# Optimization experiments

Hardware: AMD Instinct MI355X
Metric: run time of the kernel (lower is better)

## Reference

```python
import jax, jax.numpy as jnp
import numpy as np

T, B, A_DIM = 64, 128, 5
N_AGENTS, N_CAP = 8, 7
OBS_D = 64
CAP_D = N_AGENTS * N_CAP  # 56
FC, HN, TGT = 128, 128, 64
D = N_CAP + 1  # transformer model dim = 8
NH, FF, NL = 4, 64, 2
EPS = 1e-6


def _ln(x, s, b):
    m = jnp.mean(x, -1, keepdims=True)
    v = jnp.mean(jnp.square(x - m), -1, keepdims=True)
    return (x - m) * jax.lax.rsqrt(v + EPS) * s + b


def _hyper(x, w1, b1, w2, b2):
    return jax.nn.relu(x @ w1 + b1) @ w2 + b2


def setup_inputs() -> dict:
    key = jax.random.key(0)
    ks = iter(jax.random.split(key, 40))

    def rn(shape, s=0.1):
        return jax.random.normal(next(ks), shape, jnp.float32) * s

    return dict(
        hidden=jnp.zeros((B, FC), jnp.float32),
        full_obs=jax.random.normal(next(ks), (T, B, OBS_D + CAP_D), jnp.float32),
        dones=jax.random.randint(next(ks), (T, B), 0, 2, jnp.int32),
        embed_w=rn((OBS_D, FC)), embed_b=jnp.zeros((FC,), jnp.float32),
        gru_wi=rn((FC, 3 * FC)), gru_wh=rn((FC, 3 * FC)), gru_bh=jnp.zeros((3 * FC,), jnp.float32),
        tWq=rn((NL, D, D), 0.3), tWk=rn((NL, D, D), 0.3), tWv=rn((NL, D, D), 0.3), tWo=rn((NL, D, D), 0.3),
        ln1_s=jnp.ones((NL, D), jnp.float32), ln1_b=jnp.zeros((NL, D), jnp.float32),
        ffw1=rn((NL, D, FF), 0.2), ffb1=jnp.zeros((NL, FF), jnp.float32),
        ffw2=rn((NL, FF, D), 0.2), ffb2=jnp.zeros((NL, D), jnp.float32),
        ln2_s=jnp.ones((NL, D), jnp.float32), ln2_b=jnp.zeros((NL, D), jnp.float32),
        hw1_1=rn((D, HN)), hb1_1=jnp.zeros((HN,), jnp.float32), hw2_1=rn((HN, FC * TGT), 0.02), hb2_1=jnp.zeros((FC * TGT,), jnp.float32),
        hw1_2=rn((D, HN)), hb1_2=jnp.zeros((HN,), jnp.float32), hw2_2=rn((HN, TGT), 0.02), hb2_2=jnp.zeros((TGT,), jnp.float32),
        hw1_3=rn((D, HN)), hb1_3=jnp.zeros((HN,), jnp.float32), hw2_3=rn((HN, TGT * A_DIM), 0.01), hb2_3=jnp.zeros((TGT * A_DIM,), jnp.float32),
        hw1_4=rn((D, HN)), hb1_4=jnp.zeros((HN,), jnp.float32), hw2_4=rn((HN, A_DIM), 0.01), hb2_4=jnp.zeros((A_DIM,), jnp.float32),
    )


def reference(hidden, full_obs, dones, embed_w, embed_b, gru_wi, gru_wh, gru_bh,
              tWq, tWk, tWv, tWo, ln1_s, ln1_b, ffw1, ffb1, ffw2, ffb2, ln2_s, ln2_b,
              hw1_1, hb1_1, hw2_1, hb2_1, hw1_2, hb1_2, hw2_2, hb2_2,
              hw1_3, hb1_3, hw2_3, hb2_3, hw1_4, hb1_4, hw2_4, hb2_4):
    obs = full_obs[:, :, :OBS_D]          # [T,B,OBS_D]
    cap = full_obs[:, :, OBS_D:]          # [T,B,CAP_D]
    emb = jax.nn.relu(obs @ embed_w + embed_b)  # [T,B,FC]
    resets = dones.astype(bool)

    # --- GRU scan over time (flax GRUCell math: input dense no bias, hidden dense with bias) ---
    def gru_step(h, xt):
        e, d = xt
        h = jnp.where(d[:, None], 0.0, h)
        gi = e @ gru_wi                   # [B, 3*FC]
        gh = h @ gru_wh + gru_bh
        ir, iz, inn = jnp.split(gi, 3, -1)
        hr, hz, hn = jnp.split(gh, 3, -1)
        r = jax.nn.sigmoid(ir + hr)
        z = jax.nn.sigmoid(iz + hz)
        n = jnp.tanh(inn + r * hn)
        hnew = (1.0 - z) * n + z * h
        return hnew, hnew

    hidden, emb_seq = jax.lax.scan(gru_step, hidden, (emb, resets))

    # --- transformer over agents dim ---
    x = cap.reshape(T * B, N_AGENTS, N_CAP)
    flag = jnp.zeros((T * B, N_AGENTS, 1), jnp.float32).at[:, 0, 0].set(1.0)
    x = jnp.concatenate([x, flag], axis=-1)   # [N, A, D]
    hd = D // NH
    scale = 1.0 / jnp.sqrt(jnp.float32(hd))
    for l in range(NL):
        q = (x @ tWq[l]).reshape(-1, N_AGENTS, NH, hd)
        k = (x @ tWk[l]).reshape(-1, N_AGENTS, NH, hd)
        v = (x @ tWv[l]).reshape(-1, N_AGENTS, NH, hd)
        att = jax.nn.softmax(jnp.einsum('nqhd,nkhd->nhqk', q, k) * scale, axis=-1)
        o = jnp.einsum('nhqk,nkhd->nqhd', att, v).reshape(-1, N_AGENTS, D) @ tWo[l]
        # original does x = norm(attn + x); x = x + dropout(x) -> doubles x
        x = 2.0 * _ln(o + x, ln1_s[l], ln1_b[l])
        ff = jax.nn.relu(x @ ffw1[l] + ffb1[l]) @ ffw2[l] + ffb2[l]
        x = 2.0 * _ln(ff + x, ln2_s[l], ln2_b[l])
    cap_repr = jnp.mean(x, axis=1).reshape(T, B, D)

    # --- hypernetworks -> per-(t,b) weights ---
    w1 = _hyper(cap_repr, hw1_1, hb1_1, hw2_1, hb2_1).reshape(T, B, FC, TGT)
    b1 = _hyper(cap_repr, hw1_2, hb1_2, hw2_2, hb2_2).reshape(T, B, 1, TGT)
    w2 = _hyper(cap_repr, hw1_3, hb1_3, hw2_3, hb2_3).reshape(T, B, TGT, A_DIM)
    b2 = _hyper(cap_repr, hw1_4, hb1_4, hw2_4, hb2_4).reshape(T, B, 1, A_DIM)

    h1 = jax.nn.relu(emb_seq[:, :, None, :] @ w1 + b1)   # [T,B,1,TGT]
    logits = (h1 @ w2 + b2).squeeze(2)                    # [T,B,A_DIM]
    return hidden, logits
```

## Files before the change

### kernel.cpp

```cpp
#include <hip/hip_runtime.h>
#include <hip/hip_bf16.h>
#include <stdint.h>

#define TT 64
#define BB 128
#define OBSD 64
#define FOBS 120
#define FC 128
#define G3 384
#define NS 8192
#define DD 8
#define FF 64
#define HN 128
#define TGT 64
#define ADIM 5

typedef __attribute__((ext_vector_type(8))) short bf16x8;
typedef __attribute__((ext_vector_type(4))) float f32x4;

__device__ __forceinline__ float sigmoidf_(float x) { return 1.0f / (1.0f + __expf(-x)); }
__device__ __forceinline__ float tanhf_(float x) {
    float e = __expf(-2.0f * fabsf(x));
    float r = (1.0f - e) / (1.0f + e);
    return copysignf(r, x);
}
__device__ __forceinline__ unsigned short f2bf_rne(float x) {
    unsigned u = __float_as_uint(x);
    return (unsigned short)((u + 0x7fffu + ((u >> 16) & 1u)) >> 16);
}

__global__ __launch_bounds__(256) void k_embed(
    const float* __restrict__ fobs, const float* __restrict__ We,
    const float* __restrict__ be, float* __restrict__ emb)
{
    __shared__ float obs_t[64][68];
    __shared__ float W_t[64][128];
    int tid = threadIdx.x;
    int s0 = blockIdx.x * 64;
    {
        int rl = tid >> 4, e4 = tid & 15;
#pragma unroll
        for (int rr = 0; rr < 4; ++rr) {
            int r = rl + rr * 16;
            float4 v = *(const float4*)&fobs[(size_t)(s0 + r) * FOBS + e4 * 4];
            *(float4*)&obs_t[r][e4 * 4] = v;
        }
    }
#pragma unroll
    for (int i = 0; i < 8; ++i) {
        int idx = tid + i * 256;
        int e = idx >> 5, c4 = idx & 31;
        float4 v = *(const float4*)&We[(size_t)e * 128 + c4 * 4];
        *(float4*)&W_t[e][c4 * 4] = v;
    }
    __syncthreads();
    int c = tid & 127, half = tid >> 7;
    float acc[32];
    float bc = be[c];
#pragma unroll
    for (int k = 0; k < 32; ++k) acc[k] = bc;
#pragma unroll
    for (int e4 = 0; e4 < 16; ++e4) {
        float w0 = W_t[4 * e4 + 0][c], w1 = W_t[4 * e4 + 1][c];
        float w2 = W_t[4 * e4 + 2][c], w3 = W_t[4 * e4 + 3][c];
#pragma unroll
        for (int k = 0; k < 32; ++k) {
            float4 ov = *(const float4*)&obs_t[half * 32 + k][e4 * 4];
            acc[k] += ov.x * w0 + ov.y * w1 + ov.z * w2 + ov.w * w3;
        }
    }
#pragma unroll
    for (int k = 0; k < 32; ++k)
        emb[(size_t)(s0 + half * 32 + k) * FC + c] = fmaxf(acc[k], 0.0f);
}

__global__ __launch_bounds__(256) void k_gi(
    const float* __restrict__ emb, const float* __restrict__ Wi, float* __restrict__ gi)
{
    __shared__ float e_t[64][132];
    __shared__ float w_t[128 * 64];
    int tid = threadIdx.x;
    int st = blockIdx.x / 6, gt = blockIdx.x % 6;
    int s0 = st * 64, g0 = gt * 64;
#pragma unroll
    for (int i = 0; i < 8; ++i) {
        int idx = tid + i * 256;
        int r = idx >> 5, c4 = idx & 31;
        float4 v = *(const float4*)&emb[(size_t)(s0 + r) * FC + c4 * 4];
        *(float4*)&e_t[r][c4 * 4] = v;
    }
#pragma unroll
    for (int i = 0; i < 8; ++i) {
        int idx = tid + i * 256;
        int r = idx >> 4, g4 = idx & 15;
        float4 v = *(const float4*)&Wi[(size_t)r * G3 + g0 + g4 * 4];
        *(float4*)&w_t[r * 64 + g4 * 4] = v;
    }
    __syncthreads();
    int sb4 = (tid >> 4) * 4, ob4 = (tid & 15) * 4;
    float acc[4][4];
#pragma unroll
    for (int a = 0; a < 4; ++a)
#pragma unroll
        for (int b = 0; b < 4; ++b) acc[a][b] = 0.0f;
    for (int c4 = 0; c4 < 32; ++c4) {
        float4 e4[4], w4[4];
#pragma unroll
        for (int si = 0; si < 4; ++si) e4[si] = *(const float4*)&e_t[sb4 + si][c4 * 4];
#pragma unroll
        for (int cc = 0; cc < 4; ++cc) w4[cc] = *(const float4*)&w_t[(c4 * 4 + cc) * 64 + ob4];
#pragma unroll
        for (int si = 0; si < 4; ++si) {
            const float* ep = (const float*)&e4[si];
#pragma unroll
            for (int cc = 0; cc < 4; ++cc) {
                float ev = ep[cc];
                const float* wp = (const float*)&w4[cc];
                acc[si][0] += ev * wp[0];
                acc[si][1] += ev * wp[1];
                acc[si][2] += ev * wp[2];
                acc[si][3] += ev * wp[3];
            }
        }
    }
#pragma unroll
    for (int si = 0; si < 4; ++si) {
        float4 sv;
        sv.x = acc[si][0]; sv.y = acc[si][1]; sv.z = acc[si][2]; sv.w = acc[si][3];
        *(float4*)&gi[(size_t)(s0 + sb4 + si) * G3 + g0 + ob4] = sv;
    }
}

__global__ __launch_bounds__(256) void k_prepW(
    const float* __restrict__ W, unsigned short* __restrict__ W_swz)
{
    int fid = blockIdx.x * 256 + threadIdx.x;
    int lane = fid & 63;
    int nt = (fid >> 6) & 3;
    int ks = (fid >> 8) & 3;
    int j  = fid >> 10;
    int col = nt * 16 + (lane & 15);
    int kbase = ks * 32 + ((lane >> 4) * 8);
    const float* src = W + ((size_t)j * 128 + kbase) * 64 + col;
    unsigned short o[8];
#pragma unroll
    for (int i = 0; i < 8; ++i) o[i] = f2bf_rne(src[(size_t)i * 64]);
    *(uint4*)&W_swz[(size_t)fid * 8] = *(const uint4*)o;
}

__global__ __launch_bounds__(768) void k_gru(
    const float* __restrict__ gi, const float* __restrict__ Wh, const float* __restrict__ bh,
    const int* __restrict__ dones, const float* __restrict__ h0,
    float* __restrict__ emb_seq, unsigned short* __restrict__ embb,
    float* __restrict__ hid_out)
{
    __shared__ float h_lds[128];
    __shared__ float gh_lds[384];
    int b = blockIdx.x, tid = threadIdx.x;
    int col = tid >> 1, half = tid & 1;
    float W[64];
#pragma unroll
    for (int i = 0; i < 64; ++i) W[i] = Wh[(size_t)(half * 64 + i) * G3 + col];
    float bias = bh[col];
    if (tid < 128) h_lds[tid] = h0[(size_t)b * FC + tid];
    __syncthreads();
    for (int t = 0; t < TT; ++t) {
        float hs = dones[t * BB + b] ? 0.0f : 1.0f;
        float d = 0.0f;
#pragma unroll
        for (int i4 = 0; i4 < 16; ++i4) {
            float4 h4 = *(const float4*)&h_lds[half * 64 + i4 * 4];
            d += W[i4 * 4 + 0] * h4.x + W[i4 * 4 + 1] * h4.y
               + W[i4 * 4 + 2] * h4.z + W[i4 * 4 + 3] * h4.w;
        }
        d *= hs;
        d += __shfl_xor(d, 1, 64);
        if (half == 0) gh_lds[col] = d + bias;
        __syncthreads();
        if (tid < 128) {
            int c = tid;
            const float* gr = gi + ((size_t)t * BB + b) * G3;
            float r = sigmoidf_(gr[c] + gh_lds[c]);
            float z = sigmoidf_(gr[128 + c] + gh_lds[128 + c]);
            float n = tanhf_(gr[256 + c] + r * gh_lds[256 + c]);
            float hnew = (1.0f - z) * n + z * (hs * h_lds[c]);
            h_lds[c] = hnew;
            emb_seq[((size_t)t * BB + b) * FC + c] = hnew;
            embb[((size_t)t * BB + b) * FC + c] = f2bf_rne(hnew);
        }
        __syncthreads();
    }
    if (tid < 128) hid_out[(size_t)b * FC + tid] = h_lds[tid];
}

__global__ __launch_bounds__(256) void k_attn(
    const float* __restrict__ fobs,
    const float* __restrict__ tWq, const float* __restrict__ tWk,
    const float* __restrict__ tWv, const float* __restrict__ tWo,
    const float* __restrict__ ln1s, const float* __restrict__ ln1b,
    const float* __restrict__ ffw1, const float* __restrict__ ffb1,
    const float* __restrict__ ffw2, const float* __restrict__ ffb2,
    const float* __restrict__ ln2s, const float* __restrict__ ln2b,
    float* __restrict__ cap_repr)
{
    __shared__ float wq[2][8][8], wk[2][8][8], wv[2][8][8], wo[2][8][8];
    __shared__ float l1s[2][8], l1b[2][8], l2s[2][8], l2b[2][8];
    __shared__ float f1[2][8][64], fb1[2][64];
    __shared__ float f2[2][64][8], fb2w[2][8];
    __shared__ float k_l[32][8][9], v_l[32][8][9];
    int tid = threadIdx.x;
    for (int i = tid; i < 128; i += 256) {
        ((float*)wq)[i] = tWq[i]; ((float*)wk)[i] = tWk[i];
        ((float*)wv)[i] = tWv[i]; ((float*)wo)[i] = tWo[i];
        ((float*)fb1)[i] = ffb1[i];
    }
    if (tid < 16) {
        ((float*)l1s)[tid] = ln1s[tid]; ((float*)l1b)[tid] = ln1b[tid];
        ((float*)l2s)[tid] = ln2s[tid]; ((float*)l2b)[tid] = ln2b[tid];
        ((float*)fb2w)[tid] = ffb2[tid];
    }
    for (int i = tid; i < 1024; i += 256) { ((float*)f1)[i] = ffw1[i]; ((float*)f2)[i] = ffw2[i]; }
    int sl = tid >> 3, a = tid & 7;
    int s = blockIdx.x * 32 + sl;
    float x[8];
#pragma unroll
    for (int i = 0; i < 7; ++i) x[i] = fobs[(size_t)s * FOBS + OBSD + a * 7 + i];
    x[7] = (a == 0) ? 1.0f : 0.0f;
    __syncthreads();
    for (int l = 0; l < 2; ++l) {
        float q[8], k[8], v[8];
#pragma unroll
        for (int d = 0; d < 8; ++d) { q[d] = 0.f; k[d] = 0.f; v[d] = 0.f; }
#pragma unroll
        for (int e = 0; e < 8; ++e) {
            float xe = x[e];
#pragma unroll
            for (int d = 0; d < 8; ++d) {
                q[d] += xe * wq[l][e][d];
                k[d] += xe * wk[l][e][d];
                v[d] += xe * wv[l][e][d];
            }
        }
#pragma unroll
        for (int d = 0; d < 8; ++d) { k_l[sl][a][d] = k[d]; v_l[sl][a][d] = v[d]; }
        __syncthreads();
        float o[8];
#pragma unroll
        for (int h = 0; h < 4; ++h) {
            float sc[8]; float mx = -1e30f;
#pragma unroll
            for (int ka = 0; ka < 8; ++ka) {
                float sv = (q[2 * h] * k_l[sl][ka][2 * h] + q[2 * h + 1] * k_l[sl][ka][2 * h + 1])
                           * 0.70710678118654752f;
                sc[ka] = sv; mx = fmaxf(mx, sv);
            }
            float ssum = 0.f;
#pragma unroll
            for (int ka = 0; ka < 8; ++ka) { sc[ka] = __expf(sc[ka] - mx); ssum += sc[ka]; }
            float inv = 1.0f / ssum;
            float o0 = 0.f, o1 = 0.f;
#pragma unroll
            for (int ka = 0; ka < 8; ++ka) {
                float at = sc[ka] * inv;
                o0 += at * v_l[sl][ka][2 * h];
                o1 += at * v_l[sl][ka][2 * h + 1];
            }
            o[2 * h] = o0; o[2 * h + 1] = o1;
        }
        float y[8];
#pragma unroll
        for (int e = 0; e < 8; ++e) y[e] = x[e];
#pragma unroll
        for (int d = 0; d < 8; ++d) {
            float od = o[d];
#pragma unroll
            for (int e = 0; e < 8; ++e) y[e] += od * wo[l][d][e];
        }
        {
            float m = 0.f;
#pragma unroll
            for (int e = 0; e < 8; ++e) m += y[e];
            m *= 0.125f;
            float vv = 0.f;
#pragma unroll
            for (int e = 0; e < 8; ++e) { float dd = y[e] - m; vv += dd * dd; }
            vv *= 0.125f;
            float rs = rsqrtf(vv + 1e-6f);
#pragma unroll
            for (int e = 0; e < 8; ++e)
                x[e] = 2.0f * ((y[e] - m) * rs * l1s[l][e] + l1b[l][e]);
        }
        float t1[64];
#pragma unroll
        for (int f = 0; f < 64; ++f) t1[f] = 0.f;
#pragma unroll
        for (int e = 0; e < 8; ++e) {
            float xe = x[e];
#pragma unroll
            for (int f = 0; f < 64; ++f) t1[f] += xe * f1[l][e][f];
        }
        float y2[8];
#pragma unroll
        for (int e = 0; e < 8; ++e) y2[e] = x[e] + fb2w[l][e];
#pragma unroll
        for (int f = 0; f < 64; ++f) {
            float tf = fmaxf(t1[f] + fb1[l][f], 0.0f);
#pragma unroll
            for (int e = 0; e < 8; ++e) y2[e] += tf * f2[l][f][e];
        }
        {
            float m = 0.f;
#pragma unroll
            for (int e = 0; e < 8; ++e) m += y2[e];
            m *= 0.125f;
            float vv = 0.f;
#pragma unroll
            for (int e = 0; e < 8; ++e) { float dd = y2[e] - m; vv += dd * dd; }
            vv *= 0.125f;
            float rs = rsqrtf(vv + 1e-6f);
#pragma unroll
            for (int e = 0; e < 8; ++e)
                x[e] = 2.0f * ((y2[e] - m) * rs * l2s[l][e] + l2b[l][e]);
        }
        __syncthreads();
    }
#pragma unroll
    for (int e = 0; e < 8; ++e) {
        float xv = x[e];
        xv += __shfl_xor(xv, 1, 8);
        xv += __shfl_xor(xv, 2, 8);
        xv += __shfl_xor(xv, 4, 8);
        if (a == 0) cap_repr[(size_t)s * 8 + e] = xv * 0.125f;
    }
}

__global__ __launch_bounds__(256) void k_hyper(
    const float* __restrict__ cap_repr, const float* __restrict__ emb_seq,
    const float* __restrict__ hw1_1, const float* __restrict__ hb1_1,
    const float* __restrict__ hw1_2, const float* __restrict__ hb1_2,
    const float* __restrict__ hw1_3, const float* __restrict__ hb1_3,
    const float* __restrict__ hw1_4, const float* __restrict__ hb1_4,
    const float* __restrict__ hb2_1,
    const float* __restrict__ hw2_2, const float* __restrict__ hb2_2,
    const float* __restrict__ hw2_3, const float* __restrict__ hb2_3,
    const float* __restrict__ hw2_4, const float* __restrict__ hb2_4,
    float* __restrict__ hh1g, float* __restrict__ b1eff,
    float* __restrict__ w2h, float* __restrict__ b2h)
{
    __shared__ float cr[16][8];
    __shared__ float hh[4][16][132];
    __shared__ float es[16][132];
    int tid = threadIdx.x;
    int s0 = blockIdx.x * 16;
    if (tid < 128) ((float*)cr)[tid] = cap_repr[(size_t)s0 * 8 + tid];
#pragma unroll
    for (int i = 0; i < 2; ++i) {
        int idx = tid + i * 256;
        int r = idx >> 5, c4 = idx & 31;
        float4 v = *(const float4*)&emb_seq[(size_t)(s0 + r) * FC + c4 * 4];
        *(float4*)&es[r][c4 * 4] = v;
    }
    __syncthreads();
#pragma unroll
    for (int it = 0; it < 32; ++it) {
        int idx = tid + it * 256;
        int u = idx & 127;
        int sn = (idx >> 7) & 15;
        int n = idx >> 11;
        const float* w = (n == 0) ? hw1_1 : ((n == 1) ? hw1_2 : ((n == 2) ? hw1_3 : hw1_4));
        const float* bb = (n == 0) ? hb1_1 : ((n == 1) ? hb1_2 : ((n == 2) ? hb1_3 : hb1_4));
        float acc = bb[u];
#pragma unroll
        for (int e = 0; e < 8; ++e) acc += cr[sn][e] * w[e * 128 + u];
        acc = fmaxf(acc, 0.0f);
        hh[n][sn][u] = acc;
        if (n == 0) hh1g[(size_t)(s0 + sn) * 128 + u] = acc;
    }
    __syncthreads();
#pragma unroll
    for (int it = 0; it < 4; ++it) {
        int idx = tid + it * 256;
        int o = idx & 63, sn = idx >> 6;
        float acc = hb2_2[o];
        for (int j = 0; j < 128; ++j) acc += hh[1][sn][j] * hw2_2[j * 64 + o];
        for (int c = 0; c < 128; ++c) acc += es[sn][c] * hb2_1[c * 64 + o];
        b1eff[(size_t)(s0 + sn) * 64 + o] = acc;
    }
    for (int it = 0; it < 2; ++it) {
        int oa = tid + it * 256;
        if (oa < 320) {
            float acc[16];
#pragma unroll
            for (int sn = 0; sn < 16; ++sn) acc[sn] = 0.f;
            for (int j = 0; j < 128; ++j) {
                float w = hw2_3[j * 320 + oa];
#pragma unroll
                for (int sn = 0; sn < 16; ++sn) acc[sn] += hh[2][sn][j] * w;
            }
            float bb = hb2_3[oa];
#pragma unroll
            for (int sn = 0; sn < 16; ++sn) w2h[(size_t)(s0 + sn) * 320 + oa] = acc[sn] + bb;
        }
    }
    if (tid < 80) {
        int aa = tid % 5, sn = tid / 5;
        float acc = hb2_4[aa];
        for (int j = 0; j < 128; ++j) acc += hh[3][sn][j] * hw2_4[j * 5 + aa];
        b2h[(size_t)(s0 + sn) * 5 + aa] = acc;
    }
}

__global__ __launch_bounds__(256) void k_bigmm_mfma(
    const unsigned short* __restrict__ embb, const float* __restrict__ hh1g,
    const unsigned short* __restrict__ W_swz, float* __restrict__ partials)
{
    __shared__ uint4 w_lds[1024];
    __shared__ float hh1_lds[64][33];
    int tid = threadIdx.x;
    int w = tid >> 6, lane = tid & 63;
    int mt = blockIdx.x >> 2, ksp = blockIdx.x & 3;
    int s0 = mt * 64, j0 = ksp * 32;

#pragma unroll
    for (int it = 0; it < 8; ++it) {
        int idx = tid + it * 256;
        int r = idx >> 5, jj = idx & 31;
        hh1_lds[r][jj] = hh1g[(size_t)(s0 + r) * 128 + j0 + jj];
    }

    bf16x8 emb_r[2][4];
    int rbase = s0 + (w >> 1) * 32 + (lane & 15);
    int cbase = (lane >> 4) * 8;
#pragma unroll
    for (int rt = 0; rt < 2; ++rt)
#pragma unroll
        for (int ks = 0; ks < 4; ++ks)
            emb_r[rt][ks] = *(const bf16x8*)&embb[(size_t)(rbase + rt * 16) * 128 + ks * 32 + cbase];

    const uint4* Wg = (const uint4*)W_swz;
    uint4 wreg[4];
#pragma unroll
    for (int q = 0; q < 4; ++q) wreg[q] = Wg[(size_t)j0 * 1024 + q * 256 + tid];

    int nt0 = (w & 1) * 2;
    f32x4 acc[2][2];
#pragma unroll
    for (int a = 0; a < 2; ++a)
#pragma unroll
        for (int b = 0; b < 2; ++b) acc[a][b] = (f32x4){0.f, 0.f, 0.f, 0.f};

    int rl0 = (w >> 1) * 32 + 4 * (lane >> 4);
    for (int jj = 0; jj < 32; ++jj) {
        __syncthreads();
#pragma unroll
        for (int q = 0; q < 4; ++q) w_lds[q * 256 + tid] = wreg[q];
        if (jj < 31) {
#pragma unroll
            for (int q = 0; q < 4; ++q) wreg[q] = Wg[(size_t)(j0 + jj + 1) * 1024 + q * 256 + tid];
        }
        __syncthreads();
        f32x4 P00 = (f32x4){0.f, 0.f, 0.f, 0.f};
        f32x4 P01 = (f32x4){0.f, 0.f, 0.f, 0.f};
        f32x4 P10 = (f32x4){0.f, 0.f, 0.f, 0.f};
        f32x4 P11 = (f32x4){0.f, 0.f, 0.f, 0.f};
#pragma unroll
        for (int ks = 0; ks < 4; ++ks) {
            bf16x8 b0 = *(const bf16x8*)&w_lds[(ks * 4 + nt0) * 64 + lane];
            bf16x8 b1 = *(const bf16x8*)&w_lds[(ks * 4 + nt0 + 1) * 64 + lane];
            P00 = __builtin_amdgcn_mfma_f32_16x16x32_bf16(emb_r[0][ks], b0, P00, 0, 0, 0);
            P01 = __builtin_amdgcn_mfma_f32_16x16x32_bf16(emb_r[0][ks], b1, P01, 0, 0, 0);
            P10 = __builtin_amdgcn_mfma_f32_16x16x32_bf16(emb_r[1][ks], b0, P10, 0, 0, 0);
            P11 = __builtin_amdgcn_mfma_f32_16x16x32_bf16(emb_r[1][ks], b1, P11, 0, 0, 0);
        }
#pragma unroll
        for (int r = 0; r < 4; ++r) {
            float h0 = hh1_lds[rl0 + r][jj];
            float h1 = hh1_lds[rl0 + 16 + r][jj];
            acc[0][0][r] += h0 * P00[r];
            acc[0][1][r] += h0 * P01[r];
            acc[1][0][r] += h1 * P10[r];
            acc[1][1][r] += h1 * P11[r];
        }
    }
    float* pb = partials + (size_t)ksp * (NS * 64);
#pragma unroll
    for (int rt = 0; rt < 2; ++rt) {
#pragma unroll
        for (int n = 0; n < 2; ++n) {
            int colg = (w & 1) * 32 + n * 16 + (lane & 15);
#pragma unroll
            for (int r = 0; r < 4; ++r) {
                int rowg = s0 + (w >> 1) * 32 + rt * 16 + 4 * (lane >> 4) + r;
                pb[(size_t)rowg * 64 + colg] = acc[rt][n][r];
            }
        }
    }
}

__global__ __launch_bounds__(256) void k_final(
    const float* __restrict__ partials, const float* __restrict__ b1eff,
    const float* __restrict__ w2h, const float* __restrict__ b2h, float* __restrict__ out)
{
    int tid = threadIdx.x;
    int wv = tid >> 6, lane = tid & 63;
    int s = blockIdx.x * 4 + wv;
    float h1 = b1eff[(size_t)s * 64 + lane];
#pragma unroll
    for (int ks = 0; ks < 4; ++ks) h1 += partials[(size_t)ks * (NS * 64) + (size_t)s * 64 + lane];
    h1 = fmaxf(h1, 0.0f);
    float lg[5];
#pragma unroll
    for (int aa = 0; aa < 5; ++aa) lg[aa] = h1 * w2h[(size_t)s * 320 + lane * 5 + aa];
#pragma unroll
    for (int off = 32; off >= 1; off >>= 1) {
#pragma unroll
        for (int aa = 0; aa < 5; ++aa) lg[aa] += __shfl_xor(lg[aa], off, 64);
    }
    if (lane == 0) {
#pragma unroll
        for (int aa = 0; aa < 5; ++aa)
            out[16384 + (size_t)s * 5 + aa] = lg[aa] + b2h[(size_t)s * 5 + aa];
    }
}

extern "C" void kernel_launch(void* const* d_in, const int* in_sizes, int n_in,
                              void* d_out, int out_size, void* d_ws, size_t ws_size,
                              hipStream_t stream)
{
    (void)in_sizes; (void)n_in; (void)out_size; (void)ws_size;
    const float* hidden  = (const float*)d_in[0];
    const float* fobs    = (const float*)d_in[1];
    const int*   dones   = (const int*)d_in[2];
    const float* embed_w = (const float*)d_in[3];
    const float* embed_b = (const float*)d_in[4];
    const float* gru_wi  = (const float*)d_in[5];
    const float* gru_wh  = (const float*)d_in[6];
    const float* gru_bh  = (const float*)d_in[7];
    const float* tWq  = (const float*)d_in[8];
    const float* tWk  = (const float*)d_in[9];
    const float* tWv  = (const float*)d_in[10];
    const float* tWo  = (const float*)d_in[11];
    const float* ln1s = (const float*)d_in[12];
    const float* ln1b = (const float*)d_in[13];
    const float* ffw1 = (const float*)d_in[14];
    const float* ffb1 = (const float*)d_in[15];
    const float* ffw2 = (const float*)d_in[16];
    const float* ffb2 = (const float*)d_in[17];
    const float* ln2s = (const float*)d_in[18];
    const float* ln2b = (const float*)d_in[19];
    const float* hw1_1 = (const float*)d_in[20]; const float* hb1_1 = (const float*)d_in[21];
    const float* hw2_1 = (const float*)d_in[22]; const float* hb2_1 = (const float*)d_in[23];
    const float* hw1_2 = (const float*)d_in[24]; const float* hb1_2 = (const float*)d_in[25];
    const float* hw2_2 = (const float*)d_in[26]; const float* hb2_2 = (const float*)d_in[27];
    const float* hw1_3 = (const float*)d_in[28]; const float* hb1_3 = (const float*)d_in[29];
    const float* hw2_3 = (const float*)d_in[30]; const float* hb2_3 = (const float*)d_in[31];
    const float* hw1_4 = (const float*)d_in[32]; const float* hb1_4 = (const float*)d_in[33];
    const float* hw2_4 = (const float*)d_in[34]; const float* hb2_4 = (const float*)d_in[35];
    float* out = (float*)d_out;
    float* ws  = (float*)d_ws;

    float* gi      = ws;
    float* parts   = ws;
    float* emb     = gi      + 3145728;
    unsigned short* W_swz    = (unsigned short*)emb;
    unsigned short* emb_bf16 = (unsigned short*)(emb + 524288);
    float* emb_seq = emb     + 1048576;
    float* cap_rep = emb_seq + 1048576;
    float* hh1g    = cap_rep + 65536;
    float* b1eff_  = hh1g    + 1048576;
    float* w2hb    = b1eff_  + 524288;
    float* b2hb    = w2hb    + 2621440;

    k_embed<<<128, 256, 0, stream>>>(fobs, embed_w, embed_b, emb);
    k_gi<<<768, 256, 0, stream>>>(emb, gru_wi, gi);
    k_prepW<<<512, 256, 0, stream>>>(hw2_1, W_swz);
    k_gru<<<128, 768, 0, stream>>>(gi, gru_wh, gru_bh, dones, hidden, emb_seq, emb_bf16, out);
    k_attn<<<256, 256, 0, stream>>>(fobs, tWq, tWk, tWv, tWo, ln1s, ln1b,
                                    ffw1, ffb1, ffw2, ffb2, ln2s, ln2b, cap_rep);
    k_hyper<<<512, 256, 0, stream>>>(cap_rep, emb_seq,
                                     hw1_1, hb1_1, hw1_2, hb1_2, hw1_3, hb1_3, hw1_4, hb1_4,
                                     hb2_1, hw2_2, hb2_2, hw2_3, hb2_3, hw2_4, hb2_4,
                                     hh1g, b1eff_, w2hb, b2hb);
    k_bigmm_mfma<<<512, 256, 0, stream>>>(emb_bf16, hh1g, W_swz, parts);
    k_final<<<2048, 256, 0, stream>>>(parts, b1eff_, w2hb, b2hb, out);
}
```

Measured before the change: 405.9 us.

## Restructure GRU recurrence to one barrier per step with gi prefetch

The GRU kernel is remapped so each of 512 threads handles one hidden column across all three gates, with a 4-way K-split reduced by shuffles. The gate nonlinearity is fused into the same threads, which removes the gh LDS round trip and one of the two barriers per timestep. h is double-buffered in padded LDS to avoid bank conflicts, and gi/dones values are prefetched two steps ahead in registers to hide global latency on the serial path. The cost is 96 weight registers per thread and redundant gate math across the 4 lanes of each column.

New measurement: 381.4 us. 1.06x faster.

```diff
diff --git a/kernel.cpp b/kernel.cpp
--- a/kernel.cpp
+++ b/kernel.cpp
@@ -148,49 +148,79 @@
     *(uint4*)&W_swz[(size_t)fid * 8] = *(const uint4*)o;
 }
 
-__global__ __launch_bounds__(768) void k_gru(
+__global__ __launch_bounds__(512, 2) void k_gru(
     const float* __restrict__ gi, const float* __restrict__ Wh, const float* __restrict__ bh,
     const int* __restrict__ dones, const float* __restrict__ h0,
     float* __restrict__ emb_seq, unsigned short* __restrict__ embb,
     float* __restrict__ hid_out)
 {
-    __shared__ float h_lds[128];
-    __shared__ float gh_lds[384];
+    __shared__ float h_lds[2][144];
     int b = blockIdx.x, tid = threadIdx.x;
-    int col = tid >> 1, half = tid & 1;
-    float W[64];
-#pragma unroll
-    for (int i = 0; i < 64; ++i) W[i] = Wh[(size_t)(half * 64 + i) * G3 + col];
-    float bias = bh[col];
-    if (tid < 128) h_lds[tid] = h0[(size_t)b * FC + tid];
+    int c = tid >> 2, q = tid & 3;
+    int posc = (c >> 5) * 36 + (c & 31);
+
+    float W[96];
+#pragma unroll
+    for (int g = 0; g < 3; ++g)
+#pragma unroll
+        for (int i = 0; i < 32; ++i)
+            W[g * 32 + i] = Wh[(size_t)(q * 32 + i) * G3 + g * 128 + c];
+    float bq0 = bh[c], bq1 = bh[128 + c], bq2 = bh[256 + c];
+
+    if (tid < 128) h_lds[0][(tid >> 5) * 36 + (tid & 31)] = h0[(size_t)b * FC + tid];
+
+    const float* g0p = gi + ((size_t)0 * BB + b) * G3;
+    const float* g1p = gi + ((size_t)1 * BB + b) * G3;
+    float gc0 = g0p[c], gc1 = g0p[128 + c], gc2 = g0p[256 + c];
+    float n10 = g1p[c], n11 = g1p[128 + c], n12 = g1p[256 + c];
+    int dval = dones[b];
+    int dn1 = dones[BB + b];
     __syncthreads();
+
+    int cur = 0;
     for (int t = 0; t < TT; ++t) {
-        float hs = dones[t * BB + b] ? 0.0f : 1.0f;
-        float d = 0.0f;
-#pragma unroll
-        for (int i4 = 0; i4 < 16; ++i4) {
-            float4 h4 = *(const float4*)&h_lds[half * 64 + i4 * 4];
-            d += W[i4 * 4 + 0] * h4.x + W[i4 * 4 + 1] * h4.y
-               + W[i4 * 4 + 2] * h4.z + W[i4 * 4 + 3] * h4.w;
-        }
-        d *= hs;
-        d += __shfl_xor(d, 1, 64);
-        if (half == 0) gh_lds[col] = d + bias;
-        __syncthreads();
-        if (tid < 128) {
-            int c = tid;
-            const float* gr = gi + ((size_t)t * BB + b) * G3;
-            float r = sigmoidf_(gr[c] + gh_lds[c]);
-            float z = sigmoidf_(gr[128 + c] + gh_lds[128 + c]);
-            float n = tanhf_(gr[256 + c] + r * gh_lds[256 + c]);
-            float hnew = (1.0f - z) * n + z * (hs * h_lds[c]);
-            h_lds[c] = hnew;
+        int t2 = (t + 2 < TT) ? t + 2 : TT - 1;
+        const float* gp2 = gi + ((size_t)t2 * BB + b) * G3;
+        float p0 = gp2[c], p1 = gp2[128 + c], p2 = gp2[256 + c];
+        int pd = dones[t2 * BB + b];
+
+        float d0 = 0.f, d1 = 0.f, d2 = 0.f;
+        const float* hb = &h_lds[cur][q * 36];
+#pragma unroll
+        for (int i4 = 0; i4 < 8; ++i4) {
+            float4 h4 = *(const float4*)&hb[i4 * 4];
+            const float* hp = (const float*)&h4;
+#pragma unroll
+            for (int e = 0; e < 4; ++e) {
+                int i = i4 * 4 + e;
+                d0 += W[i] * hp[e];
+                d1 += W[32 + i] * hp[e];
+                d2 += W[64 + i] * hp[e];
+            }
+        }
+        d0 += __shfl_xor(d0, 1, 64); d0 += __shfl_xor(d0, 2, 64);
+        d1 += __shfl_xor(d1, 1, 64); d1 += __shfl_xor(d1, 2, 64);
+        d2 += __shfl_xor(d2, 1, 64); d2 += __shfl_xor(d2, 2, 64);
+
+        float hs = dval ? 0.0f : 1.0f;
+        float hold = h_lds[cur][posc];
+        float r = sigmoidf_(gc0 + d0 * hs + bq0);
+        float z = sigmoidf_(gc1 + d1 * hs + bq1);
+        float n = tanhf_(gc2 + r * (d2 * hs + bq2));
+        float hnew = (1.0f - z) * n + z * (hs * hold);
+
+        if (q == 0) {
+            h_lds[cur ^ 1][posc] = hnew;
             emb_seq[((size_t)t * BB + b) * FC + c] = hnew;
             embb[((size_t)t * BB + b) * FC + c] = f2bf_rne(hnew);
         }
+        gc0 = n10; gc1 = n11; gc2 = n12;
+        n10 = p0;  n11 = p1;  n12 = p2;
+        dval = dn1; dn1 = pd;
         __syncthreads();
-    }
-    if (tid < 128) hid_out[(size_t)b * FC + tid] = h_lds[tid];
+        cur ^= 1;
+    }
+    if (tid < 128) hid_out[(size_t)b * FC + tid] = h_lds[cur][(tid >> 5) * 36 + (tid & 31)];
 }
 
 __global__ __launch_bounds__(256) void k_attn(
@@ -574,7 +604,7 @@
     k_embed<<<128, 256, 0, stream>>>(fobs, embed_w, embed_b, emb);
     k_gi<<<768, 256, 0, stream>>>(emb, gru_wi, gi);
     k_prepW<<<512, 256, 0, stream>>>(hw2_1, W_swz);
-    k_gru<<<128, 768, 0, stream>>>(gi, gru_wh, gru_bh, dones, hidden, emb_seq, emb_bf16, out);
+    k_gru<<<128, 512, 0, stream>>>(gi, gru_wh, gru_bh, dones, hidden, emb_seq, emb_bf16, out);
     k_attn<<<256, 256, 0, stream>>>(fobs, tWq, tWk, tWv, tWo, ln1s, ln1b,
                                     ffw1, ffb1, ffw2, ffb2, ln2s, ln2b, cap_rep);
     k_hyper<<<512, 256, 0, stream>>>(cap_rep, emb_seq,
```
